# Kernel tuning notes

Measured on AMD Instinct MI355X. Metric: run time of the kernel, lower is better.

The kernel has to match this reference:

```python
import jax, jax.numpy as jnp
import numpy as np

B, M, PAST, FUT, NPRED, D = 512, 32768, 8, 12, 20, 48


def _gru_step(h, x, w_ih, w_hh, b_ih, b_hh):
    # torch GRU cell: gates ordered [r, z, n]
    gi = x @ w_ih.T + b_ih
    gh = h @ w_hh.T + b_hh
    ir, iz, inn = jnp.split(gi, 3, axis=-1)
    hr, hz, hn = jnp.split(gh, 3, axis=-1)
    r = jax.nn.sigmoid(ir + hr)
    z = jax.nn.sigmoid(iz + hz)
    n = jnp.tanh(inn + r * hn)
    return (1.0 - z) * n + z * h


def setup_inputs() -> dict:
    key = jax.random.key(0)
    ks = jax.random.split(key, 16)
    f32 = jnp.float32
    def rn(k, shp, sc):
        return (jax.random.normal(k, shp, dtype=f32) * sc)
    return {
        "past": jax.random.normal(ks[0], (B, PAST, 2), dtype=f32),
        "obs_traj": jax.random.normal(ks[1], (B, PAST, 2), dtype=f32),
        "conv_w": rn(ks[2], (D, 2, 3), 0.3),
        "conv_b": jnp.zeros((D,), f32),
        "enc_w_ih": rn(ks[3], (3 * D, D), 0.1),
        "enc_w_hh": rn(ks[4], (3 * D, D), 0.1),
        "enc_b_ih": jnp.zeros((3 * D,), f32),
        "enc_b_hh": jnp.zeros((3 * D,), f32),
        "memory_past": jax.random.normal(ks[5], (M, D), dtype=f32),
        "memory_fut": jax.random.normal(ks[6], (M, D), dtype=f32),
        "Wq": rn(ks[7], (D, D), 0.1), "bq": jnp.zeros((D,), f32),
        "Wk": rn(ks[8], (D, D), 0.1), "bk": jnp.zeros((D,), f32),
        "Wv": rn(ks[9], (D, D), 0.1), "bv": jnp.zeros((D,), f32),
        "dec_w_ih": rn(ks[10], (6 * D, 2 * D), 0.1),
        "dec_w_hh": rn(ks[11], (6 * D, 2 * D), 0.1),
        "dec_b_ih": jnp.zeros((6 * D,), f32),
        "dec_b_hh": jnp.zeros((6 * D,), f32),
        "fc_w": rn(ks[12], (2, 2 * D), 0.1),
        "fc_b": jnp.zeros((2,), f32),
    }


def reference(past, obs_traj, conv_w, conv_b, enc_w_ih, enc_w_hh, enc_b_ih, enc_b_hh,
              memory_past, memory_fut, Wq, bq, Wk, bk, Wv, bv,
              dec_w_ih, dec_w_hh, dec_b_ih, dec_b_hh, fc_w, fc_b):
    b = past.shape[0]
    # --- past encoder: Conv1d(2,48,3,pad=1) + ReLU, then GRU(48,48) ---
    x = jnp.transpose(past, (0, 2, 1))                     # [B,2,T]
    emb = jax.lax.conv_general_dilated(
        x, conv_w, (1,), [(1, 1)], dimension_numbers=("NCH", "OIH", "NCH"))
    emb = jax.nn.relu(emb + conv_b[None, :, None])         # [B,48,T]
    emb = jnp.transpose(emb, (2, 0, 1))                    # [T,B,48] for scan

    def enc_step(h, x_t):
        return _gru_step(h, x_t, enc_w_ih, enc_w_hh, enc_b_ih, enc_b_hh), None
    state_past, _ = jax.lax.scan(enc_step, jnp.zeros((b, D), past.dtype), emb)  # [B,48]

    # --- iterative refinement: 20 rounds of attention over the full memory ---
    # Lin_K/Lin_V are applied to the same (full) banks every iteration -> hoist.
    K = memory_past @ Wk.T + bk                            # [M,48]
    V = memory_fut @ Wv.T + bv                             # [M,48]

    def irm_step(c, _):
        q = c @ Wq.T + bq                                  # [B,48]
        a = jax.nn.softmax(q @ K.T, axis=-1)               # [B,M], scale=1.0
        att = a @ V                                        # [B,48]
        return q + att, att
    _, atts = jax.lax.scan(irm_step, state_past, None, length=NPRED)  # [20,B,48]
    pred = jnp.transpose(atts, (1, 0, 2)).reshape(-1, D)   # [B*20,48] (b-major)

    # --- GRU(96,96) decoder, future_len steps, input only at t=0 ---
    n = b * NPRED
    present = jnp.repeat(obs_traj[:, -1], NPRED, axis=0)   # [B*20,2]
    sp = jnp.repeat(state_past, NPRED, axis=0)             # [B*20,48]
    info = jnp.concatenate([sp, pred], axis=1)             # [B*20,96]
    xs = jnp.concatenate(
        [info[None], jnp.zeros((FUT - 1, n, 2 * D), info.dtype)], axis=0)

    def dec_step(carry, x_t):
        h, pres = carry
        h = _gru_step(h, x_t, dec_w_ih, dec_w_hh, dec_b_ih, dec_b_hh)
        pres = pres + (h @ fc_w.T + fc_b)
        return (h, pres), pres
    _, coords = jax.lax.scan(
        dec_step, (jnp.zeros((n, 2 * D), info.dtype), present), xs)  # [FUT,B*20,2]

    prediction = jnp.transpose(coords, (1, 0, 2)).reshape(b, NPRED, FUT, 2)
    return prediction
```

## Files before the change

kernel.cpp:

```cpp
#include <hip/hip_runtime.h>

typedef unsigned short u16;
typedef unsigned int u32;
typedef __attribute__((ext_vector_type(8))) short short8v;
typedef __attribute__((ext_vector_type(4))) float f32x4;

#define GLD_LDS(g, l) __builtin_amdgcn_global_load_lds( \
    (const __attribute__((address_space(1))) void*)(g), \
    (__attribute__((address_space(3))) void*)(l), 16, 0, 0)

#define LOG2E 1.44269504f

__device__ __forceinline__ u16 f2bf(float f){
  union { float f; u32 u; } v; v.f = f;
  u32 r = v.u + 0x7FFFu + ((v.u >> 16) & 1u);
  return (u16)(r >> 16);
}
__device__ __forceinline__ float bf2f(u16 h){
  union { u32 u; float f; } v; v.u = ((u32)h) << 16;
  return v.f;
}
__device__ __forceinline__ u32 pk2(float a, float b){
  union { float f; u32 u; } x, y; x.f = a; y.f = b;
  return __builtin_amdgcn_perm(y.u + 0x8000u, x.u + 0x8000u, 0x07060302u);
}
__device__ __forceinline__ float sigm(float x){ return 1.f/(1.f+__expf(-x)); }
__device__ __forceinline__ float tanh_fast(float x){ return 1.f - 2.f/(1.f+__expf(2.f*x)); }

__global__ void prep_kernel(const float* dih, const float* dhh,
    const float* eih, const float* ehh, const float* wq, const float* wk, const float* wv,
    u16* Dih, u16* Dhh, u16* Eih, u16* Ehh, u16* Qf, u16* Kf, u16* Vf)
{
  int idx = blockIdx.x*256 + threadIdx.x;
// ... 161 lines not shown
      short8v aF1 = *(const short8v*)&smf[ln*72 + 32 + qd*8];
      f32x4 k3[3], v3[3];
      #pragma unroll
      for (int nt = 0; nt < 3; ++nt){ k3[nt] = zf; v3[nt] = zf; }
      #pragma unroll
      for (int nt = 0; nt < 3; ++nt){
        k3[nt] = __builtin_amdgcn_mfma_f32_16x16x32_bf16(aP0, *(const short8v*)&sWkF[((nt*2+0)*4+qd)*128 + ln*8], k3[nt], 0,0,0);
        k3[nt] = __builtin_amdgcn_mfma_f32_16x16x32_bf16(aP1, *(const short8v*)&sWkF[((nt*2+1)*4+qd)*128 + ln*8], k3[nt], 0,0,0);
        v3[nt] = __builtin_amdgcn_mfma_f32_16x16x32_bf16(aF0, *(const short8v*)&sWvF[((nt*2+0)*4+qd)*128 + ln*8], v3[nt], 0,0,0);
        v3[nt] = __builtin_amdgcn_mfma_f32_16x16x32_bf16(aF1, *(const short8v*)&sWvF[((nt*2+1)*4+qd)*128 + ln*8], v3[nt], 0,0,0);
      }
      for (int i = lane; i < 128; i += 64) ((u32*)sKT)[(wid*16 + (i>>3))*32 + 24 + (i&7)] = 0;
      #pragma unroll
      for (int nt = 0; nt < 3; ++nt)
        #pragma unroll
        for (int r = 0; r < 4; ++r){
          int keyl = wid*16 + qd*4 + r, d = nt*16 + ln;
          sKT[keyl*64 + d] = f2bf(k3[nt][r] + bkv[nt]);
          sVT[d*72 + keyl] = f2bf(v3[nt][r] + bvv[nt]);
        }
      __syncthreads();
      for (int i = tid; i < 512; i += 256)
        *(uint4*)((char*)(Kb + (size_t)tile*64*64) + i*16) = *(const uint4*)((char*)sKT + i*16);
      for (int i = tid; i < 384; i += 256){
        int d = i>>3, sub = i&7;
        *(uint4*)((char*)(Vc + ((size_t)((tile*64)>>8)*48 + d)*256 + ((tile*64)&255)) + sub*16)
            = *(const uint4*)((char*)sVT + d*144 + sub*16);
      }
      __syncthreads();
    }
  }
}

__global__ __launch_bounds__(256, 1) void iter_kernel(int mode, int it,
    const u16* qbB, const u16* Kb, const u16* Vc, const u16* WqF, const float* bq,
    const float* qfP, float* qfC, float* pred,
    const float* mP, const float* lP, const float* aP,
    float* mC, float* lC, float* aC)
{
  __shared__ __align__(16) char SMEM[55936];
  u16*   sQ  = (u16*)(SMEM + 45056);
  float* sWc = (float*)(SMEM + 49152);
  float* sLg = (float*)(SMEM + 51200);
  u16*   sCb = (u16*)(SMEM + 51332);
  const int tid = threadIdx.x, bx = blockIdx.x;
  const int wid = tid>>6, lane = tid&63, qd = lane>>4, ln = lane&15;
  const int rg = bx>>4, ch = bx&15;
  const int rowbase = rg*32;
  f32x4 zf = {0.f,0.f,0.f,0.f};

  if (mode == 1){
    float* sRed = (float*)SMEM;
    {
      int row = tid>>3, jj = tid&7, grow = rowbase + row;
      float m0 = mP[grow*16 + jj*2], m1 = mP[grow*16 + jj*2+1];
      float l0 = lP[grow*16 + jj*2], l1 = lP[grow*16 + jj*2+1];
      float mg = fmaxf(m0, m1);
      #pragma unroll
      for (int k = 1; k < 8; k <<= 1) mg = fmaxf(mg, __shfl_xor(mg, k));
      float w0 = exp2f(m0 - mg), w1 = exp2f(m1 - mg);
      float wl = w0*l0 + w1*l1;
      #pragma unroll
      for (int k = 1; k < 8; k <<= 1) wl += __shfl_xor(wl, k);
      sWc[row*16 + jj*2] = w0; sWc[row*16 + jj*2+1] = w1;
      if (jj == 0) sLg[row] = wl;
    }
    __syncthreads();
    {
      f32x4 accv[6];
      #pragma unroll
      for (int i = 0; i < 6; ++i) accv[i] = zf;
      #pragma unroll
      for (int ci = 0; ci < 4; ++ci){
        int c = wid*4 + ci;
        const f32x4* slab = (const f32x4*)(aP + ((size_t)c*512 + rowbase)*48);
        #pragma unroll
        for (int i = 0; i < 6; ++i){
          f32x4 v = slab[i*64 + lane];
          int rr = (i*64 + lane)/12;
          float w = sWc[rr*16 + c];
          accv[i][0] += w*v[0]; accv[i][1] += w*v[1];
          accv[i][2] += w*v[2]; accv[i][3] += w*v[3];
        }
      }
      float* red = sRed + wid*1536;
      #pragma unroll
      for (int i = 0; i < 6; ++i)
        *(f32x4*)&red[(i*64 + lane)*4] = accv[i];
    }
    __syncthreads();
    {
      int row = tid>>3, jj = tid&7, grow = rowbase + row;
      float lg = sLg[row];
      int base = row*48 + jj*6;
      #pragma unroll
      for (int d6 = 0; d6 < 6; ++d6){
        int d = jj*6 + d6;
        float s = sRed[base+d6] + sRed[1536+base+d6] + sRed[3072+base+d6] + sRed[4608+base+d6];
        float a = s / lg;
        if (ch == 0) pred[(size_t)(grow*20 + (it-1))*48 + d] = a;
        sCb[row*72 + d] = f2bf(qfP[grow*48 + d] + a);
      }
      ((u32*)&sCb[row*72 + 48])[jj] = 0;
    }
    __syncthreads();
    if (wid < 2){
      short8v ac0 = *(const short8v*)&sCb[(wid*16+ln)*72 + qd*8];
      short8v ac1 = *(const short8v*)&sCb[(wid*16+ln)*72 + 32 + qd*8];
      f32x4 q3[3];
      #pragma unroll
      for (int nt = 0; nt < 3; ++nt){
        q3[nt] = zf;
        q3[nt] = __builtin_amdgcn_mfma_f32_16x16x32_bf16(ac0, *(const short8v*)&WqF[((nt*2+0)*4+qd)*128 + ln*8], q3[nt], 0,0,0);
        q3[nt] = __builtin_amdgcn_mfma_f32_16x16x32_bf16(ac1, *(const short8v*)&WqF[((nt*2+1)*4+qd)*128 + ln*8], q3[nt], 0,0,0);
      }
      #pragma unroll
      for (int nt = 0; nt < 3; ++nt)
        #pragma unroll
        for (int r = 0; r < 4; ++r){
          int lr = wid*16 + qd*4 + r, d = nt*16 + ln;
          float v = q3[nt][r] + bq[d];
          if (ch == 0) qfC[(rowbase + lr)*48 + d] = v;
          sQ[lr*64 + d] = f2bf(v * LOG2E);
        }
    } else {
      for (int i = tid-128; i < 256; i += 128){
        int r2 = i>>3, p = i&7;
        ((u32*)&sQ[r2*64 + 48])[p] = 0;
      }
    }
    __syncthreads();
  } else {
    const u32* src = (const u32*)(qbB + rowbase*64);
    ((u32*)sQ)[tid]       = src[tid];
    ((u32*)sQ)[256 + tid] = src[256 + tid];
    ((u32*)sQ)[512 + tid] = src[512 + tid];
    ((u32*)sQ)[768 + tid] = src[768 + tid];
    __syncthreads();
  }

  const int wslice = ch*2048 + wid*512;
  u16* sp8 = (u16*)(SMEM + 26624);
  short8v aq[2][2];
  #pragma unroll
  for (int rt = 0; rt < 2; ++rt)
    #pragma unroll
    for (int kc = 0; kc < 2; ++kc)
      aq[rt][kc] = *(const short8v*)&sQ[(rt*16+ln)*64 + kc*32 + qd*8];
  f32x4 acc[2][3];
  #pragma unroll
  for (int rt = 0; rt < 2; ++rt) for (int dt = 0; dt < 3; ++dt) acc[rt][dt] = zf;
  float mrun[2] = {-3.0e38f, -3.0e38f}, lrun[2] = {0.f, 0.f};
  u16* spb[2] = { sp8 + (wid*2+0)*1152, sp8 + (wid*2+1)*1152 };

  #pragma unroll
  for (int kt = 0; kt < 8; ++kt){
    const int tb = wslice + kt*64;
    const u16* kb = Kb + (size_t)tb*64;
    const u16* vb = Vc + (size_t)(tb>>8)*48*256 + (tb & 255);
    short8v kf[4][2], vf[2][3];
    #pragma unroll
    for (int nt = 0; nt < 4; ++nt)
      #pragma unroll
      for (int kc = 0; kc < 2; ++kc)
        kf[nt][kc] = *(const short8v*)&kb[(nt*16+ln)*64 + kc*32 + qd*8];
    #pragma unroll
    for (int kc = 0; kc < 2; ++kc)
      #pragma unroll
      for (int dt = 0; dt < 3; ++dt)
        vf[kc][dt] = *(const short8v*)&vb[(dt*16+ln)*256 + kc*32 + qd*8];
    f32x4 s[2][4];
    #pragma unroll
    for (int rt = 0; rt < 2; ++rt)
      #pragma unroll
      for (int nt = 0; nt < 4; ++nt){
        f32x4 z = zf;
        z = __builtin_amdgcn_mfma_f32_16x16x32_bf16(kf[nt][0], aq[rt][0], z, 0,0,0);
        z = __builtin_amdgcn_mfma_f32_16x16x32_bf16(kf[nt][1], aq[rt][1], z, 0,0,0);
        s[rt][nt] = z;
      }
    #pragma unroll
    for (int rt = 0; rt < 2; ++rt){
      float vmax = fmaxf(fmaxf(fmaxf(s[rt][0][0], s[rt][0][1]), fmaxf(s[rt][0][2], s[rt][0][3])),
                   fmaxf(fmaxf(s[rt][1][0], s[rt][1][1]), fmaxf(s[rt][1][2], s[rt][1][3])));
      vmax = fmaxf(vmax, fmaxf(fmaxf(fmaxf(s[rt][2][0], s[rt][2][1]), fmaxf(s[rt][2][2], s[rt][2][3])),
                   fmaxf(fmaxf(s[rt][3][0], s[rt][3][1]), fmaxf(s[rt][3][2], s[rt][3][3]))));
      vmax = fmaxf(vmax, __shfl_xor(vmax, 16));
      vmax = fmaxf(vmax, __shfl_xor(vmax, 32));
      float mnew = fmaxf(mrun[rt], vmax);
      float alpha = exp2f(mrun[rt] - mnew);
      mrun[rt] = mnew;
      u16* sp = spb[rt];
      float lsum = 0.f;
      #pragma unroll
      for (int nt = 0; nt < 4; ++nt){
        float p0 = exp2f(s[rt][nt][0]-mnew), p1 = exp2f(s[rt][nt][1]-mnew);
        float p2 = exp2f(s[rt][nt][2]-mnew), p3 = exp2f(s[rt][nt][3]-mnew);
        lsum += (p0+p1)+(p2+p3);
        uint2 pk; pk.x = pk2(p0,p1); pk.y = pk2(p2,p3);
        *(uint2*)&sp[ln*72 + nt*16 + qd*4] = pk;
      }
      lsum += __shfl_xor(lsum, 16);
      lsum += __shfl_xor(lsum, 32);
      lrun[rt] = lrun[rt]*alpha + lsum;
      #pragma unroll
      for (int dt = 0; dt < 3; ++dt){
        acc[rt][dt][0] *= alpha; acc[rt][dt][1] *= alpha;
        acc[rt][dt][2] *= alpha; acc[rt][dt][3] *= alpha;
      }
      short8v pb0 = *(const short8v*)&sp[ln*72 + qd*8];
      short8v pb1 = *(const short8v*)&sp[ln*72 + 32 + qd*8];
      #pragma unroll
      for (int dt = 0; dt < 3; ++dt){
        acc[rt][dt] = __builtin_amdgcn_mfma_f32_16x16x32_bf16(vf[0][dt], pb0, acc[rt][dt], 0,0,0);
        acc[rt][dt] = __builtin_amdgcn_mfma_f32_16x16x32_bf16(vf[1][dt], pb1, acc[rt][dt], 0,0,0);
      }
    }
  }
  __syncthreads();
  float* sMg = (float*)SMEM;
  #pragma unroll
  for (int rt = 0; rt < 2; ++rt)
    #pragma unroll
    for (int dt = 0; dt < 3; ++dt)
      #pragma unroll
      for (int r = 0; r < 4; ++r)
        sMg[wid*1600 + (rt*16+ln)*50 + dt*16 + qd*4 + r] = acc[rt][dt][r];
  if (lane < 16){
    sMg[wid*1600 + ln*50 + 48] = mrun[0]; sMg[wid*1600 + ln*50 + 49] = lrun[0];
    sMg[wid*1600 + (16+ln)*50 + 48] = mrun[1]; sMg[wid*1600 + (16+ln)*50 + 49] = lrun[1];
  }
  __syncthreads();
  {
    int row = tid>>3, jj = tid&7, grow = rowbase + row;
    float m0 = sMg[row*50+48], m1 = sMg[1600+row*50+48];
    float m2 = sMg[3200+row*50+48], m3 = sMg[4800+row*50+48];
    float mg = fmaxf(fmaxf(m0,m1), fmaxf(m2,m3));
    float e0 = exp2f(m0-mg), e1 = exp2f(m1-mg), e2 = exp2f(m2-mg), e3 = exp2f(m3-mg);
    float lg = e0*sMg[row*50+49] + e1*sMg[1600+row*50+49]
             + e2*sMg[3200+row*50+49] + e3*sMg[4800+row*50+49];
    if (jj == 0){ mC[grow*16 + ch] = mg; lC[grow*16 + ch] = lg; }
    int d0 = jj*6;
    #pragma unroll
    for (int d6 = 0; d6 < 6; ++d6){
      int d = d0 + d6;
      aC[((size_t)ch*512 + grow)*48 + d] =
          e0*sMg[row*50+d] + e1*sMg[1600+row*50+d]
        + e2*sMg[3200+row*50+d] + e3*sMg[4800+row*50+d];
    }
  }
}

__global__ __launch_bounds__(384, 1) void dec_kernel(
    const u16* Dihf, const u16* Dhhf, const float* b_ih, const float* b_hh,
    const float* stateP, const float* pred, const float* obs,
    const float* mF, const float* lF, const float* aF,
    const float* fc_w, const float* fc_b, float* out)
{
  __shared__ __align__(16) u16 sx[2][16*106];
  __shared__ float sPx[2][6][16], sPy[2][6][16];
  const int tid = threadIdx.x, bx = blockIdx.x;
  const int wid = tid>>6, lane = tid&63, qd = lane>>4, ln = lane&15;
  const int rw = bx*16;
  f32x4 zf = {0.f,0.f,0.f,0.f};

  for (int i = tid; i < 1536; i += 384){
    int r = i/96, k = i - r*96;
    int row = rw + r, b20 = row/20;
    float v = (k < 48) ? stateP[b20*48 + k] : pred[(size_t)row*48 + (k-48)];
    sx[0][r*106 + k] = f2bf(v);
  }
  if (tid < 48){
    int r19 = (19 - (rw % 20)) % 20;
    if (r19 < 16){
      int b = (rw + r19)/20;
      float mg = -3.0e38f, mv[16];
      #pragma unroll
      for (int c = 0; c < 16; ++c){ mv[c] = mF[b*16 + c]; mg = fmaxf(mg, mv[c]); }
      float num = 0.f, den = 0.f;
      #pragma unroll
      for (int c = 0; c < 16; ++c){
        float w = exp2f(mv[c] - mg);
        den += w * lF[b*16 + c];
        num += w * aF[((size_t)c*512 + b)*48 + tid];
      }
      sx[0][r19*106 + 48 + tid] = f2bf(num/den);
    }
  }
  short8v whh[3][3];
  #pragma unroll
  for (int g = 0; g < 3; ++g)
    #pragma unroll
    for (int kc = 0; kc < 3; ++kc)
      whh[g][kc] = *(const short8v*)&Dhhf[(((g*6+wid)*3+kc)*4+qd)*128 + ln*8];
  const int d = wid*16 + ln;
  float biR=b_ih[d], biZ=b_ih[96+d], biN=b_ih[192+d];
  float bhR=b_hh[d], bhZ=b_hh[96+d], bhN=b_hh[192+d];
  float fw0=fc_w[d], fw1=fc_w[96+d];
  float hold[4] = {0.f,0.f,0.f,0.f};
  float fcb0 = fc_b[0], fcb1 = fc_b[1];
  float pres0 = 0.f, pres1 = 0.f;
  if (wid == 0 && lane < 16){
    int b20 = (rw + lane)/20;
    pres0 = obs[b20*16 + 14];
    pres1 = obs[b20*16 + 15];
  }
  __syncthreads();

  #pragma unroll 1
  for (int t = 0; t < 12; ++t){
    const u16* sr = sx[t&1];
    u16* sw = sx[(t+1)&1];
    short8v xa0 = *(const short8v*)&sr[ln*106 + qd*8];
    short8v xa1 = *(const short8v*)&sr[ln*106 + 32 + qd*8];
    short8v xa2 = *(const short8v*)&sr[ln*106 + 64 + qd*8];
    f32x4 acc[3] = {zf, zf, zf};
    if (t == 0){
      #pragma unroll
      for (int g = 0; g < 3; ++g){
        int nt = g*6 + wid;
        acc[g] = __builtin_amdgcn_mfma_f32_16x16x32_bf16(xa0, *(const short8v*)&Dihf[((nt*3+0)*4+qd)*128 + ln*8], acc[g], 0,0,0);
        acc[g] = __builtin_amdgcn_mfma_f32_16x16x32_bf16(xa1, *(const short8v*)&Dihf[((nt*3+1)*4+qd)*128 + ln*8], acc[g], 0,0,0);
        acc[g] = __builtin_amdgcn_mfma_f32_16x16x32_bf16(xa2, *(const short8v*)&Dihf[((nt*3+2)*4+qd)*128 + ln*8], acc[g], 0,0,0);
      }
    } else {
      #pragma unroll
      for (int g = 0; g < 3; ++g){
        acc[g] = __builtin_amdgcn_mfma_f32_16x16x32_bf16(xa0, whh[g][0], acc[g], 0,0,0);
        acc[g] = __builtin_amdgcn_mfma_f32_16x16x32_bf16(xa1, whh[g][1], acc[g], 0,0,0);
        acc[g] = __builtin_amdgcn_mfma_f32_16x16x32_bf16(xa2, whh[g][2], acc[g], 0,0,0);
      }
    }
    float px[4], py[4];
    #pragma unroll
    for (int r = 0; r < 4; ++r){
      float rr = sigm(acc[0][r] + biR + bhR);
      float zz = sigm(acc[1][r] + biZ + bhZ);
      float nn = (t == 0) ? tanh_fast(acc[2][r] + biN + rr*bhN)
                          : tanh_fast(biN + rr*(acc[2][r] + bhN));
      float hv = (1.f-zz)*nn + zz*hold[r];
      hold[r] = hv;
      sw[(qd*4+r)*106 + d] = f2bf(hv);
      px[r] = fw0*hv;
      py[r] = fw1*hv;
    }
    #pragma unroll
    for (int msk = 8; msk >= 1; msk >>= 1)
      #pragma unroll
      for (int r = 0; r < 4; ++r){
        px[r] += __shfl_xor(px[r], msk);
        py[r] += __shfl_xor(py[r], msk);
      }
    if (ln == 0){
      #pragma unroll
      for (int r = 0; r < 4; ++r){
        sPx[t&1][wid][qd*4+r] = px[r];
        sPy[t&1][wid][qd*4+r] = py[r];
      }
    }
    __syncthreads();
    if (wid == 0 && lane < 16){
      float fx = 0.f, fy = 0.f;
      #pragma unroll
      for (int w = 0; w < 6; ++w){ fx += sPx[t&1][w][lane]; fy += sPy[t&1][w][lane]; }
      pres0 += fx + fcb0;
      pres1 += fy + fcb1;
      out[((size_t)(rw + lane)*12 + t)*2 + 0] = pres0;
      out[((size_t)(rw + lane)*12 + t)*2 + 1] = pres1;
    }
  }
}

extern "C" void kernel_launch(void* const* d_in, const int* in_sizes, int n_in,
                              void* d_out, int out_size, void* d_ws, size_t ws_size,
                              hipStream_t stream)
{
  const float* past        = (const float*)d_in[0];
  const float* obs         = (const float*)d_in[1];
  const float* conv_w      = (const float*)d_in[2];
  const float* conv_b      = (const float*)d_in[3];
  const float* enc_w_ih    = (const float*)d_in[4];
  const float* enc_w_hh    = (const float*)d_in[5];
  const float* enc_b_ih    = (const float*)d_in[6];
  const float* enc_b_hh    = (const float*)d_in[7];
  const float* memory_past = (const float*)d_in[8];
  const float* memory_fut  = (const float*)d_in[9];
  const float* Wq = (const float*)d_in[10];
  const float* bq = (const float*)d_in[11];
  const float* Wk = (const float*)d_in[12];
  const float* bk = (const float*)d_in[13];
  const float* Wv = (const float*)d_in[14];
  const float* bv = (const float*)d_in[15];
  const float* dec_w_ih = (const float*)d_in[16];
  const float* dec_w_hh = (const float*)d_in[17];
  const float* dec_b_ih = (const float*)d_in[18];
  const float* dec_b_hh = (const float*)d_in[19];
  const float* fc_w = (const float*)d_in[20];
  const float* fc_b = (const float*)d_in[21];
  float* out = (float*)d_out;

  char* ws = (char*)d_ws;
  size_t off = 0;
  auto alloc = [&](size_t bytes){ void* p = ws + off; off += (bytes + 255) & ~(size_t)255; return p; };
  float* stateP = (float*)alloc(512*48*4);
  float* qfA    = (float*)alloc(512*48*4);
  float* qfB    = (float*)alloc(512*48*4);
  u16*   qbB    = (u16*)alloc(512*64*2);
  float* mB[2], *lB[2], *aB[2];
  for (int i = 0; i < 2; ++i){
    mB[i] = (float*)alloc(512*16*4);
    lB[i] = (float*)alloc(512*16*4);
    aB[i] = (float*)alloc((size_t)512*16*48*4);
  }
  float* pred = (float*)alloc((size_t)10240*48*4);
  u16*   Kb   = (u16*)alloc((size_t)32768*64*2);
  u16*   Vc   = (u16*)alloc((size_t)32768*48*2);
  u16*   Dihf = (u16*)alloc(27648*2);
  u16*   Dhhf = (u16*)alloc(27648*2);
  u16*   EihF = (u16*)alloc(9216*2);
  u16*   EhhF = (u16*)alloc(9216*2);
  u16*   WqF  = (u16*)alloc(3072*2);
  u16*   WkF  = (u16*)alloc(3072*2);
  u16*   WvF  = (u16*)alloc(3072*2);
  float* qbuf[2] = { qfA, qfB };

  prep_kernel<<<324, 256, 0, stream>>>(dec_w_ih, dec_w_hh, enc_w_ih, enc_w_hh,
                                       Wq, Wk, Wv, Dihf, Dhhf, EihF, EhhF, WqF, WkF, WvF);

  setup_kernel<<<512, 256, 0, stream>>>(
      past, conv_w, conv_b, enc_b_ih, enc_b_hh, memory_past, memory_fut,
      bq, bk, bv, EihF, EhhF, WqF, WkF, WvF,
      stateP, qfA, qbB, Kb, Vc);

  iter_kernel<<<256, 256, 0, stream>>>(0, 0, qbB, Kb, Vc, WqF, bq,
      qfA, qfA, pred, mB[1], lB[1], aB[1], mB[0], lB[0], aB[0]);
  for (int it = 1; it < 20; ++it){
    int pv = (it-1)&1, cu = it&1;
    iter_kernel<<<256, 256, 0, stream>>>(1, it, qbB, Kb, Vc, WqF, bq,
        qbuf[pv], qbuf[cu], pred, mB[pv], lB[pv], aB[pv], mB[cu], lB[cu], aB[cu]);
  }

  dec_kernel<<<640, 384, 0, stream>>>(Dihf, Dhhf, dec_b_ih, dec_b_hh,
      stateP, pred, obs, mB[1], lB[1], aB[1], fc_w, fc_b, out);
}
```

Before: 628.7 us.

## Run decoder GRU with one wavefront per block and remap attention chunk order

The decoder kernel moves from six wavefronts per 16-row block, which needed shared-memory reduction of the fc projection and a second sync, to a single wavefront that computes all 18 gate tiles itself. The fc reduction and trajectory accumulation now stay in registers. Weights are read from global memory every step instead of being cached in registers, and each block does six times the serial MFMA work with fewer waves for latency hiding. Separately, the iteration kernel's chunk index is permuted across block IDs, likely to change how blocks are spread over XCDs or caches.

```diff
diff --git a/kernel.cpp b/kernel.cpp
--- a/kernel.cpp
+++ b/kernel.cpp
@@ -239,7 +239,8 @@
   u16*   sCb = (u16*)(SMEM + 51332);
   const int tid = threadIdx.x, bx = blockIdx.x;
   const int wid = tid>>6, lane = tid&63, qd = lane>>4, ln = lane&15;
-  const int rg = bx>>4, ch = bx&15;
+  const int ch = (bx&7)*2 + ((bx>>3)&1);
+  const int rg = bx>>4;
   const int rowbase = rg*32;
   f32x4 zf = {0.f,0.f,0.f,0.f};
 
@@ -445,26 +446,25 @@
   }
 }
 
-__global__ __launch_bounds__(384, 1) void dec_kernel(
+__global__ __launch_bounds__(64) void dec_kernel(
     const u16* Dihf, const u16* Dhhf, const float* b_ih, const float* b_hh,
     const float* stateP, const float* pred, const float* obs,
     const float* mF, const float* lF, const float* aF,
     const float* fc_w, const float* fc_b, float* out)
 {
   __shared__ __align__(16) u16 sx[2][16*106];
-  __shared__ float sPx[2][6][16], sPy[2][6][16];
-  const int tid = threadIdx.x, bx = blockIdx.x;
-  const int wid = tid>>6, lane = tid&63, qd = lane>>4, ln = lane&15;
+  const int lane = threadIdx.x, bx = blockIdx.x;
+  const int qd = lane>>4, ln = lane&15;
   const int rw = bx*16;
   f32x4 zf = {0.f,0.f,0.f,0.f};
 
-  for (int i = tid; i < 1536; i += 384){
+  for (int i = lane; i < 1536; i += 64){
     int r = i/96, k = i - r*96;
     int row = rw + r, b20 = row/20;
     float v = (k < 48) ? stateP[b20*48 + k] : pred[(size_t)row*48 + (k-48)];
     sx[0][r*106 + k] = f2bf(v);
   }
-  if (tid < 48){
+  if (lane < 48){
     int r19 = (19 - (rw % 20)) % 20;
     if (r19 < 16){
       int b = (rw + r19)/20;
@@ -476,28 +476,29 @@
       for (int c = 0; c < 16; ++c){
         float w = exp2f(mv[c] - mg);
         den += w * lF[b*16 + c];
-        num += w * aF[((size_t)c*512 + b)*48 + tid];
-      }
-      sx[0][r19*106 + 48 + tid] = f2bf(num/den);
-    }
-  }
-  short8v whh[3][3];
+        num += w * aF[((size_t)c*512 + b)*48 + lane];
+      }
+      sx[0][r19*106 + 48 + lane] = f2bf(num/den);
+    }
+  }
+  float biR[6],biZ[6],biN[6],bhR[6],bhZ[6],bhN[6],fw0[6],fw1[6];
   #pragma unroll
-  for (int g = 0; g < 3; ++g)
-    #pragma unroll
-    for (int kc = 0; kc < 3; ++kc)
-      whh[g][kc] = *(const short8v*)&Dhhf[(((g*6+wid)*3+kc)*4+qd)*128 + ln*8];
-  const int d = wid*16 + ln;
-  float biR=b_ih[d], biZ=b_ih[96+d], biN=b_ih[192+d];
-  float bhR=b_hh[d], bhZ=b_hh[96+d], bhN=b_hh[192+d];
-  float fw0=fc_w[d], fw1=fc_w[96+d];
-  float hold[4] = {0.f,0.f,0.f,0.f};
+  for (int i = 0; i < 6; ++i){
+    int d = i*16 + ln;
+    biR[i]=b_ih[d]; biZ[i]=b_ih[96+d]; biN[i]=b_ih[192+d];
+    bhR[i]=b_hh[d]; bhZ[i]=b_hh[96+d]; bhN[i]=b_hh[192+d];
+    fw0[i]=fc_w[d]; fw1[i]=fc_w[96+d];
+  }
+  float hold[6][4];
+  #pragma unroll
+  for (int i = 0; i < 6; ++i) for (int r = 0; r < 4; ++r) hold[i][r] = 0.f;
   float fcb0 = fc_b[0], fcb1 = fc_b[1];
-  float pres0 = 0.f, pres1 = 0.f;
-  if (wid == 0 && lane < 16){
-    int b20 = (rw + lane)/20;
-    pres0 = obs[b20*16 + 14];
-    pres1 = obs[b20*16 + 15];
+  float pres0[4], pres1[4];
+  #pragma unroll
+  for (int r = 0; r < 4; ++r){
+    int b20 = (rw + qd*4 + r)/20;
+    pres0[r] = obs[b20*16 + 14];
+    pres1[r] = obs[b20*16 + 15];
   }
   __syncthreads();
 
@@ -508,36 +509,32 @@
     short8v xa0 = *(const short8v*)&sr[ln*106 + qd*8];
     short8v xa1 = *(const short8v*)&sr[ln*106 + 32 + qd*8];
     short8v xa2 = *(const short8v*)&sr[ln*106 + 64 + qd*8];
-    f32x4 acc[3] = {zf, zf, zf};
-    if (t == 0){
-      #pragma unroll
-      for (int g = 0; g < 3; ++g){
-        int nt = g*6 + wid;
-        acc[g] = __builtin_amdgcn_mfma_f32_16x16x32_bf16(xa0, *(const short8v*)&Dihf[((nt*3+0)*4+qd)*128 + ln*8], acc[g], 0,0,0);
-        acc[g] = __builtin_amdgcn_mfma_f32_16x16x32_bf16(xa1, *(const short8v*)&Dihf[((nt*3+1)*4+qd)*128 + ln*8], acc[g], 0,0,0);
-        acc[g] = __builtin_amdgcn_mfma_f32_16x16x32_bf16(xa2, *(const short8v*)&Dihf[((nt*3+2)*4+qd)*128 + ln*8], acc[g], 0,0,0);
-      }
-    } else {
-      #pragma unroll
-      for (int g = 0; g < 3; ++g){
-        acc[g] = __builtin_amdgcn_mfma_f32_16x16x32_bf16(xa0, whh[g][0], acc[g], 0,0,0);
-        acc[g] = __builtin_amdgcn_mfma_f32_16x16x32_bf16(xa1, whh[g][1], acc[g], 0,0,0);
-        acc[g] = __builtin_amdgcn_mfma_f32_16x16x32_bf16(xa2, whh[g][2], acc[g], 0,0,0);
-      }
-    }
-    float px[4], py[4];
-    #pragma unroll
-    for (int r = 0; r < 4; ++r){
-      float rr = sigm(acc[0][r] + biR + bhR);
-      float zz = sigm(acc[1][r] + biZ + bhZ);
-      float nn = (t == 0) ? tanh_fast(acc[2][r] + biN + rr*bhN)
-                          : tanh_fast(biN + rr*(acc[2][r] + bhN));
-      float hv = (1.f-zz)*nn + zz*hold[r];
-      hold[r] = hv;
-      sw[(qd*4+r)*106 + d] = f2bf(hv);
-      px[r] = fw0*hv;
-      py[r] = fw1*hv;
-    }
+    const u16* W = (t == 0) ? Dihf : Dhhf;
+    f32x4 acc[18];
+    #pragma unroll
+    for (int i = 0; i < 18; ++i) acc[i] = zf;
+    #pragma unroll
+    for (int nt = 0; nt < 18; ++nt){
+      acc[nt] = __builtin_amdgcn_mfma_f32_16x16x32_bf16(xa0, *(const short8v*)&W[((nt*3+0)*4+qd)*128 + ln*8], acc[nt], 0,0,0);
+      acc[nt] = __builtin_amdgcn_mfma_f32_16x16x32_bf16(xa1, *(const short8v*)&W[((nt*3+1)*4+qd)*128 + ln*8], acc[nt], 0,0,0);
+      acc[nt] = __builtin_amdgcn_mfma_f32_16x16x32_bf16(xa2, *(const short8v*)&W[((nt*3+2)*4+qd)*128 + ln*8], acc[nt], 0,0,0);
+    }
+    float px[4] = {0,0,0,0}, py[4] = {0,0,0,0};
+    #pragma unroll
+    for (int r = 0; r < 4; ++r)
+      #pragma unroll
+      for (int i = 0; i < 6; ++i){
+        int d = i*16 + ln;
+        float rr = sigm(acc[i][r]   + biR[i] + bhR[i]);
+        float zz = sigm(acc[i+6][r] + biZ[i] + bhZ[i]);
+        float nn = (t == 0) ? tanh_fast(acc[i+12][r] + biN[i] + rr*bhN[i])
+                            : tanh_fast(biN[i] + rr*(acc[i+12][r] + bhN[i]));
+        float hv = (1.f-zz)*nn + zz*hold[i][r];
+        hold[i][r] = hv;
+        sw[(qd*4+r)*106 + d] = f2bf(hv);
+        px[r] += fw0[i]*hv;
+        py[r] += fw1[i]*hv;
+      }
     #pragma unroll
     for (int msk = 8; msk >= 1; msk >>= 1)
       #pragma unroll
@@ -545,23 +542,20 @@
         px[r] += __shfl_xor(px[r], msk);
         py[r] += __shfl_xor(py[r], msk);
       }
+    #pragma unroll
+    for (int r = 0; r < 4; ++r){
+      pres0[r] += px[r] + fcb0;
+      pres1[r] += py[r] + fcb1;
+    }
     if (ln == 0){
       #pragma unroll
       for (int r = 0; r < 4; ++r){
-        sPx[t&1][wid][qd*4+r] = px[r];
-        sPy[t&1][wid][qd*4+r] = py[r];
+        int row = rw + qd*4 + r;
+        out[((size_t)row*12 + t)*2 + 0] = pres0[r];
+        out[((size_t)row*12 + t)*2 + 1] = pres1[r];
       }
     }
     __syncthreads();
-    if (wid == 0 && lane < 16){
-      float fx = 0.f, fy = 0.f;
-      #pragma unroll
-      for (int w = 0; w < 6; ++w){ fx += sPx[t&1][w][lane]; fy += sPy[t&1][w][lane]; }
-      pres0 += fx + fcb0;
-      pres1 += fy + fcb1;
-      out[((size_t)(rw + lane)*12 + t)*2 + 0] = pres0;
-      out[((size_t)(rw + lane)*12 + t)*2 + 1] = pres1;
-    }
   }
 }
 
@@ -634,6 +628,6 @@
         qbuf[pv], qbuf[cu], pred, mB[pv], lB[pv], aB[pv], mB[cu], lB[cu], aB[cu]);
   }
 
-  dec_kernel<<<640, 384, 0, stream>>>(Dihf, Dhhf, dec_b_ih, dec_b_hh,
+  dec_kernel<<<640, 64, 0, stream>>>(Dihf, Dhhf, dec_b_ih, dec_b_hh,
       stateP, pred, obs, mB[1], lB[1], aB[1], fc_w, fc_b, out);
 }
```

New measurement: 639.0 us. No clear change (+1.6%).

## Fuse 20 attention iteration launches into one cooperative kernel with grid sync

Applied to the files above, without the earlier changes.

Replaces the 20 back-to-back iter_kernel launches with a single cooperative launch that loops over iterations and uses grid-wide sync between them. The query state now stays in shared memory across iterations. The goal is to remove per-launch overhead and launch gaps. A fallback path runs the per-iteration launches if the cooperative launch fails. It also changes the dec_kernel LDS row stride from 106 to 104 and drops its min-blocks launch bound, which may affect bank conflicts and occupancy.

```diff
diff --git a/kernel.cpp b/kernel.cpp
--- a/kernel.cpp
+++ b/kernel.cpp
@@ -1,4 +1,7 @@
 #include <hip/hip_runtime.h>
+#include <hip/hip_cooperative_groups.h>
+
+namespace cg = cooperative_groups;
 
 typedef unsigned short u16;
 typedef unsigned int u32;
@@ -226,232 +229,251 @@
   }
 }
 
-__global__ __launch_bounds__(256, 1) void iter_kernel(int mode, int it,
-    const u16* qbB, const u16* Kb, const u16* Vc, const u16* WqF, const float* bq,
-    const float* qfP, float* qfC, float* pred,
-    const float* mP, const float* lP, const float* aP,
-    float* mC, float* lC, float* aC)
+__global__ __launch_bounds__(256, 1) void iter_kernel(int it0, int it1,
+    const u16* Kb, const u16* Vc, const u16* WqF, const float* bq,
+    const float* qfIn, float* qfA, float* qfB, float* pred,
+    float* m0b, float* l0b, float* a0b, float* m1b, float* l1b, float* a1b)
 {
-  __shared__ __align__(16) char SMEM[55936];
+  __shared__ __align__(16) char SMEM[62080];
   u16*   sQ  = (u16*)(SMEM + 45056);
   float* sWc = (float*)(SMEM + 49152);
   float* sLg = (float*)(SMEM + 51200);
   u16*   sCb = (u16*)(SMEM + 51332);
+  float* sQf = (float*)(SMEM + 55936);
   const int tid = threadIdx.x, bx = blockIdx.x;
   const int wid = tid>>6, lane = tid&63, qd = lane>>4, ln = lane&15;
   const int rg = bx>>4, ch = bx&15;
   const int rowbase = rg*32;
   f32x4 zf = {0.f,0.f,0.f,0.f};
 
-  if (mode == 1){
-    float* sRed = (float*)SMEM;
-    {
-      int row = tid>>3, jj = tid&7, grow = rowbase + row;
-      float m0 = mP[grow*16 + jj*2], m1 = mP[grow*16 + jj*2+1];
-      float l0 = lP[grow*16 + jj*2], l1 = lP[grow*16 + jj*2+1];
-      float mg = fmaxf(m0, m1);
-      #pragma unroll
-      for (int k = 1; k < 8; k <<= 1) mg = fmaxf(mg, __shfl_xor(mg, k));
-      float w0 = exp2f(m0 - mg), w1 = exp2f(m1 - mg);
-      float wl = w0*l0 + w1*l1;
-      #pragma unroll
-      for (int k = 1; k < 8; k <<= 1) wl += __shfl_xor(wl, k);
-      sWc[row*16 + jj*2] = w0; sWc[row*16 + jj*2+1] = w1;
-      if (jj == 0) sLg[row] = wl;
+  for (int i = tid; i < 1536; i += 256){
+    float v = qfIn[rowbase*48 + i];
+    sQf[i] = v;
+    int row = i/48, d = i - row*48;
+    sQ[row*64 + d] = f2bf(v * LOG2E);
+  }
+  { int r2 = tid>>3, p = tid&7; ((u32*)sQ)[r2*32 + 24 + p] = 0; }
+  __syncthreads();
+
+  #pragma unroll 1
+  for (int it = it0; it < it1; ++it){
+    const float* mP = (it&1) ? m0b : m1b;
+    const float* lP = (it&1) ? l0b : l1b;
+    const float* aP = (it&1) ? a0b : a1b;
+    float* mC = (it&1) ? m1b : m0b;
+    float* lC = (it&1) ? l1b : l0b;
+    float* aC = (it&1) ? a1b : a0b;
+    float* qOut = (it&1) ? qfB : qfA;
+
+    if (it > 0){
+      float* sRed = (float*)SMEM;
+      {
+        int row = tid>>3, jj = tid&7, grow = rowbase + row;
+        float m0 = mP[grow*16 + jj*2], m1 = mP[grow*16 + jj*2+1];
+        float l0 = lP[grow*16 + jj*2], l1 = lP[grow*16 + jj*2+1];
+        float mg = fmaxf(m0, m1);
+        #pragma unroll
+        for (int k = 1; k < 8; k <<= 1) mg = fmaxf(mg, __shfl_xor(mg, k));
+        float w0 = exp2f(m0 - mg), w1 = exp2f(m1 - mg);
+        float wl = w0*l0 + w1*l1;
+        #pragma unroll
+        for (int k = 1; k < 8; k <<= 1) wl += __shfl_xor(wl, k);
+        sWc[row*16 + jj*2] = w0; sWc[row*16 + jj*2+1] = w1;
+        if (jj == 0) sLg[row] = wl;
+      }
+      __syncthreads();
+      {
+        f32x4 accv[6];
+        #pragma unroll
+        for (int i = 0; i < 6; ++i) accv[i] = zf;
+        #pragma unroll
+        for (int ci = 0; ci < 4; ++ci){
+          int c = wid*4 + ci;
+          const f32x4* slab = (const f32x4*)(aP + ((size_t)c*512 + rowbase)*48);
+          #pragma unroll
+          for (int i = 0; i < 6; ++i){
+            f32x4 v = slab[i*64 + lane];
+            int rr = (i*64 + lane)/12;
+            float w = sWc[rr*16 + c];
+            accv[i][0] += w*v[0]; accv[i][1] += w*v[1];
+            accv[i][2] += w*v[2]; accv[i][3] += w*v[3];
+          }
+        }
+        float* red = sRed + wid*1536;
+        #pragma unroll
+        for (int i = 0; i < 6; ++i)
+          *(f32x4*)&red[(i*64 + lane)*4] = accv[i];
+      }
+      __syncthreads();
+      {
+        int row = tid>>3, jj = tid&7, grow = rowbase + row;
+        float lg = sLg[row];
+        int base = row*48 + jj*6;
+        #pragma unroll
+        for (int d6 = 0; d6 < 6; ++d6){
+          int d = jj*6 + d6;
+          float s = sRed[base+d6] + sRed[1536+base+d6] + sRed[3072+base+d6] + sRed[4608+base+d6];
+          float a = s / lg;
+          if (ch == 0) pred[(size_t)(grow*20 + (it-1))*48 + d] = a;
+          sCb[row*72 + d] = f2bf(sQf[row*48 + d] + a);
+        }
+        ((u32*)&sCb[row*72 + 48])[jj] = 0;
+      }
+      __syncthreads();
+      if (wid < 2){
+        short8v ac0 = *(const short8v*)&sCb[(wid*16+ln)*72 + qd*8];
+        short8v ac1 = *(const short8v*)&sCb[(wid*16+ln)*72 + 32 + qd*8];
+        f32x4 q3[3];
+        #pragma unroll
+        for (int nt = 0; nt < 3; ++nt){
+          q3[nt] = zf;
+          q3[nt] = __builtin_amdgcn_mfma_f32_16x16x32_bf16(ac0, *(const short8v*)&WqF[((nt*2+0)*4+qd)*128 + ln*8], q3[nt], 0,0,0);
+          q3[nt] = __builtin_amdgcn_mfma_f32_16x16x32_bf16(ac1, *(const short8v*)&WqF[((nt*2+1)*4+qd)*128 + ln*8], q3[nt], 0,0,0);
+        }
+        #pragma unroll
+        for (int nt = 0; nt < 3; ++nt)
+          #pragma unroll
+          for (int r = 0; r < 4; ++r){
+            int lr = wid*16 + qd*4 + r, d = nt*16 + ln;
+            float v = q3[nt][r] + bq[d];
+            sQf[lr*48 + d] = v;
+            if (ch == 0) qOut[(rowbase + lr)*48 + d] = v;
+            sQ[lr*64 + d] = f2bf(v * LOG2E);
+          }
+      } else {
+        for (int i = tid-128; i < 256; i += 128){
+          int r2 = i>>3, p = i&7;
+          ((u32*)&sQ[r2*64 + 48])[p] = 0;
+        }
+      }
+      __syncthreads();
+    }
+
+    const int wslice = ch*2048 + wid*512;
+    u16* sp8 = (u16*)(SMEM + 26624);
+    short8v aq[2][2];
+    #pragma unroll
+    for (int rt = 0; rt < 2; ++rt)
+      #pragma unroll
+      for (int kc = 0; kc < 2; ++kc)
+        aq[rt][kc] = *(const short8v*)&sQ[(rt*16+ln)*64 + kc*32 + qd*8];
+    f32x4 acc[2][3];
+    #pragma unroll
+    for (int rt = 0; rt < 2; ++rt) for (int dt = 0; dt < 3; ++dt) acc[rt][dt] = zf;
+    float mrun[2] = {-3.0e38f, -3.0e38f}, lrun[2] = {0.f, 0.f};
+    u16* spb[2] = { sp8 + (wid*2+0)*1152, sp8 + (wid*2+1)*1152 };
+
+    #pragma unroll
+    for (int kt = 0; kt < 8; ++kt){
+      const int tb = wslice + kt*64;
+      const u16* kb = Kb + (size_t)tb*64;
+      const u16* vb = Vc + (size_t)(tb>>8)*48*256 + (tb & 255);
+      short8v kf[4][2], vf[2][3];
+      #pragma unroll
+      for (int nt = 0; nt < 4; ++nt)
+        #pragma unroll
+        for (int kc = 0; kc < 2; ++kc)
+          kf[nt][kc] = *(const short8v*)&kb[(nt*16+ln)*64 + kc*32 + qd*8];
+      #pragma unroll
+      for (int kc = 0; kc < 2; ++kc)
+        #pragma unroll
+        for (int dt = 0; dt < 3; ++dt)
+          vf[kc][dt] = *(const short8v*)&vb[(dt*16+ln)*256 + kc*32 + qd*8];
+      f32x4 s[2][4];
+      #pragma unroll
+      for (int rt = 0; rt < 2; ++rt)
+        #pragma unroll
+        for (int nt = 0; nt < 4; ++nt){
+          f32x4 z = zf;
+          z = __builtin_amdgcn_mfma_f32_16x16x32_bf16(kf[nt][0], aq[rt][0], z, 0,0,0);
+          z = __builtin_amdgcn_mfma_f32_16x16x32_bf16(kf[nt][1], aq[rt][1], z, 0,0,0);
+          s[rt][nt] = z;
+        }
+      #pragma unroll
+      for (int rt = 0; rt < 2; ++rt){
+        float vmax = fmaxf(fmaxf(fmaxf(s[rt][0][0], s[rt][0][1]), fmaxf(s[rt][0][2], s[rt][0][3])),
+                     fmaxf(fmaxf(s[rt][1][0], s[rt][1][1]), fmaxf(s[rt][1][2], s[rt][1][3])));
+        vmax = fmaxf(vmax, fmaxf(fmaxf(fmaxf(s[rt][2][0], s[rt][2][1]), fmaxf(s[rt][2][2], s[rt][2][3])),
+                     fmaxf(fmaxf(s[rt][3][0], s[rt][3][1]), fmaxf(s[rt][3][2], s[rt][3][3]))));
+        vmax = fmaxf(vmax, __shfl_xor(vmax, 16));
+        vmax = fmaxf(vmax, __shfl_xor(vmax, 32));
+        float mnew = fmaxf(mrun[rt], vmax);
+        float alpha = exp2f(mrun[rt] - mnew);
+        mrun[rt] = mnew;
+        u16* sp = spb[rt];
+        float lsum = 0.f;
+        #pragma unroll
+        for (int nt = 0; nt < 4; ++nt){
+          float p0 = exp2f(s[rt][nt][0]-mnew), p1 = exp2f(s[rt][nt][1]-mnew);
+          float p2 = exp2f(s[rt][nt][2]-mnew), p3 = exp2f(s[rt][nt][3]-mnew);
+          lsum += (p0+p1)+(p2+p3);
+          uint2 pk; pk.x = pk2(p0,p1); pk.y = pk2(p2,p3);
+          *(uint2*)&sp[ln*72 + nt*16 + qd*4] = pk;
+        }
+        lsum += __shfl_xor(lsum, 16);
+        lsum += __shfl_xor(lsum, 32);
+        lrun[rt] = lrun[rt]*alpha + lsum;
+        #pragma unroll
+        for (int dt = 0; dt < 3; ++dt){
+          acc[rt][dt][0] *= alpha; acc[rt][dt][1] *= alpha;
+          acc[rt][dt][2] *= alpha; acc[rt][dt][3] *= alpha;
+        }
+        short8v pb0 = *(const short8v*)&sp[ln*72 + qd*8];
+        short8v pb1 = *(const short8v*)&sp[ln*72 + 32 + qd*8];
+        #pragma unroll
+        for (int dt = 0; dt < 3; ++dt){
+          acc[rt][dt] = __builtin_amdgcn_mfma_f32_16x16x32_bf16(vf[0][dt], pb0, acc[rt][dt], 0,0,0);
+          acc[rt][dt] = __builtin_amdgcn_mfma_f32_16x16x32_bf16(vf[1][dt], pb1, acc[rt][dt], 0,0,0);
+        }
+      }
     }
     __syncthreads();
-    {
-      f32x4 accv[6];
-      #pragma unroll
-      for (int i = 0; i < 6; ++i) accv[i] = zf;
-      #pragma unroll
-      for (int ci = 0; ci < 4; ++ci){
-        int c = wid*4 + ci;
-        const f32x4* slab = (const f32x4*)(aP + ((size_t)c*512 + rowbase)*48);
-        #pragma unroll
-        for (int i = 0; i < 6; ++i){
-          f32x4 v = slab[i*64 + lane];
-          int rr = (i*64 + lane)/12;
-          float w = sWc[rr*16 + c];
-          accv[i][0] += w*v[0]; accv[i][1] += w*v[1];
-          accv[i][2] += w*v[2]; accv[i][3] += w*v[3];
-        }
-      }
-      float* red = sRed + wid*1536;
-      #pragma unroll
-      for (int i = 0; i < 6; ++i)
-        *(f32x4*)&red[(i*64 + lane)*4] = accv[i];
+    float* sMg = (float*)SMEM;
+    #pragma unroll
+    for (int rt = 0; rt < 2; ++rt)
+      #pragma unroll
+      for (int dt = 0; dt < 3; ++dt)
+        #pragma unroll
+        for (int r = 0; r < 4; ++r)
+          sMg[wid*1600 + (rt*16+ln)*50 + dt*16 + qd*4 + r] = acc[rt][dt][r];
+    if (lane < 16){
+      sMg[wid*1600 + ln*50 + 48] = mrun[0]; sMg[wid*1600 + ln*50 + 49] = lrun[0];
+      sMg[wid*1600 + (16+ln)*50 + 48] = mrun[1]; sMg[wid*1600 + (16+ln)*50 + 49] = lrun[1];
     }
     __syncthreads();
     {
       int row = tid>>3, jj = tid&7, grow = rowbase + row;
-      float lg = sLg[row];
-      int base = row*48 + jj*6;
+      float m0 = sMg[row*50+48], m1 = sMg[1600+row*50+48];
+      float m2 = sMg[3200+row*50+48], m3 = sMg[4800+row*50+48];
+      float mg = fmaxf(fmaxf(m0,m1), fmaxf(m2,m3));
+      float e0 = exp2f(m0-mg), e1 = exp2f(m1-mg), e2 = exp2f(m2-mg), e3 = exp2f(m3-mg);
+      float lg = e0*sMg[row*50+49] + e1*sMg[1600+row*50+49]
+               + e2*sMg[3200+row*50+49] + e3*sMg[4800+row*50+49];
+      if (jj == 0){ mC[grow*16 + ch] = mg; lC[grow*16 + ch] = lg; }
+      int d0 = jj*6;
       #pragma unroll
       for (int d6 = 0; d6 < 6; ++d6){
-        int d = jj*6 + d6;
-        float s = sRed[base+d6] + sRed[1536+base+d6] + sRed[3072+base+d6] + sRed[4608+base+d6];
-        float a = s / lg;
-        if (ch == 0) pred[(size_t)(grow*20 + (it-1))*48 + d] = a;
-        sCb[row*72 + d] = f2bf(qfP[grow*48 + d] + a);
-      }
-      ((u32*)&sCb[row*72 + 48])[jj] = 0;
+        int d = d0 + d6;
+        aC[((size_t)ch*512 + grow)*48 + d] =
+            e0*sMg[row*50+d] + e1*sMg[1600+row*50+d]
+          + e2*sMg[3200+row*50+d] + e3*sMg[4800+row*50+d];
+      }
     }
     __syncthreads();
-    if (wid < 2){
-      short8v ac0 = *(const short8v*)&sCb[(wid*16+ln)*72 + qd*8];
-      short8v ac1 = *(const short8v*)&sCb[(wid*16+ln)*72 + 32 + qd*8];
-      f32x4 q3[3];
-      #pragma unroll
-      for (int nt = 0; nt < 3; ++nt){
-        q3[nt] = zf;
-        q3[nt] = __builtin_amdgcn_mfma_f32_16x16x32_bf16(ac0, *(const short8v*)&WqF[((nt*2+0)*4+qd)*128 + ln*8], q3[nt], 0,0,0);
-        q3[nt] = __builtin_amdgcn_mfma_f32_16x16x32_bf16(ac1, *(const short8v*)&WqF[((nt*2+1)*4+qd)*128 + ln*8], q3[nt], 0,0,0);
-      }
-      #pragma unroll
-      for (int nt = 0; nt < 3; ++nt)
-        #pragma unroll
-        for (int r = 0; r < 4; ++r){
-          int lr = wid*16 + qd*4 + r, d = nt*16 + ln;
-          float v = q3[nt][r] + bq[d];
-          if (ch == 0) qfC[(rowbase + lr)*48 + d] = v;
-          sQ[lr*64 + d] = f2bf(v * LOG2E);
-        }
-    } else {
-      for (int i = tid-128; i < 256; i += 128){
-        int r2 = i>>3, p = i&7;
-        ((u32*)&sQ[r2*64 + 48])[p] = 0;
-      }
-    }
-    __syncthreads();
-  } else {
-    const u32* src = (const u32*)(qbB + rowbase*64);
-    ((u32*)sQ)[tid]       = src[tid];
-    ((u32*)sQ)[256 + tid] = src[256 + tid];
-    ((u32*)sQ)[512 + tid] = src[512 + tid];
-    ((u32*)sQ)[768 + tid] = src[768 + tid];
-    __syncthreads();
-  }
-
-  const int wslice = ch*2048 + wid*512;
-  u16* sp8 = (u16*)(SMEM + 26624);
-  short8v aq[2][2];
-  #pragma unroll
-  for (int rt = 0; rt < 2; ++rt)
-    #pragma unroll
-    for (int kc = 0; kc < 2; ++kc)
-      aq[rt][kc] = *(const short8v*)&sQ[(rt*16+ln)*64 + kc*32 + qd*8];
-  f32x4 acc[2][3];
-  #pragma unroll
-  for (int rt = 0; rt < 2; ++rt) for (int dt = 0; dt < 3; ++dt) acc[rt][dt] = zf;
-  float mrun[2] = {-3.0e38f, -3.0e38f}, lrun[2] = {0.f, 0.f};
-  u16* spb[2] = { sp8 + (wid*2+0)*1152, sp8 + (wid*2+1)*1152 };
-
-  #pragma unroll
-  for (int kt = 0; kt < 8; ++kt){
-    const int tb = wslice + kt*64;
-    const u16* kb = Kb + (size_t)tb*64;
-    const u16* vb = Vc + (size_t)(tb>>8)*48*256 + (tb & 255);
-    short8v kf[4][2], vf[2][3];
-    #pragma unroll
-    for (int nt = 0; nt < 4; ++nt)
-      #pragma unroll
-      for (int kc = 0; kc < 2; ++kc)
-        kf[nt][kc] = *(const short8v*)&kb[(nt*16+ln)*64 + kc*32 + qd*8];
-    #pragma unroll
-    for (int kc = 0; kc < 2; ++kc)
-      #pragma unroll
-      for (int dt = 0; dt < 3; ++dt)
-        vf[kc][dt] = *(const short8v*)&vb[(dt*16+ln)*256 + kc*32 + qd*8];
-    f32x4 s[2][4];
-    #pragma unroll
-    for (int rt = 0; rt < 2; ++rt)
-      #pragma unroll
-      for (int nt = 0; nt < 4; ++nt){
-        f32x4 z = zf;
-        z = __builtin_amdgcn_mfma_f32_16x16x32_bf16(kf[nt][0], aq[rt][0], z, 0,0,0);
-        z = __builtin_amdgcn_mfma_f32_16x16x32_bf16(kf[nt][1], aq[rt][1], z, 0,0,0);
-        s[rt][nt] = z;
-      }
-    #pragma unroll
-    for (int rt = 0; rt < 2; ++rt){
-      float vmax = fmaxf(fmaxf(fmaxf(s[rt][0][0], s[rt][0][1]), fmaxf(s[rt][0][2], s[rt][0][3])),
-                   fmaxf(fmaxf(s[rt][1][0], s[rt][1][1]), fmaxf(s[rt][1][2], s[rt][1][3])));
-      vmax = fmaxf(vmax, fmaxf(fmaxf(fmaxf(s[rt][2][0], s[rt][2][1]), fmaxf(s[rt][2][2], s[rt][2][3])),
-                   fmaxf(fmaxf(s[rt][3][0], s[rt][3][1]), fmaxf(s[rt][3][2], s[rt][3][3]))));
-      vmax = fmaxf(vmax, __shfl_xor(vmax, 16));
-      vmax = fmaxf(vmax, __shfl_xor(vmax, 32));
-      float mnew = fmaxf(mrun[rt], vmax);
-      float alpha = exp2f(mrun[rt] - mnew);
-      mrun[rt] = mnew;
-      u16* sp = spb[rt];
-      float lsum = 0.f;
-      #pragma unroll
-      for (int nt = 0; nt < 4; ++nt){
-        float p0 = exp2f(s[rt][nt][0]-mnew), p1 = exp2f(s[rt][nt][1]-mnew);
-        float p2 = exp2f(s[rt][nt][2]-mnew), p3 = exp2f(s[rt][nt][3]-mnew);
-        lsum += (p0+p1)+(p2+p3);
-        uint2 pk; pk.x = pk2(p0,p1); pk.y = pk2(p2,p3);
-        *(uint2*)&sp[ln*72 + nt*16 + qd*4] = pk;
-      }
-      lsum += __shfl_xor(lsum, 16);
-      lsum += __shfl_xor(lsum, 32);
-      lrun[rt] = lrun[rt]*alpha + lsum;
-      #pragma unroll
-      for (int dt = 0; dt < 3; ++dt){
-        acc[rt][dt][0] *= alpha; acc[rt][dt][1] *= alpha;
-        acc[rt][dt][2] *= alpha; acc[rt][dt][3] *= alpha;
-      }
-      short8v pb0 = *(const short8v*)&sp[ln*72 + qd*8];
-      short8v pb1 = *(const short8v*)&sp[ln*72 + 32 + qd*8];
-      #pragma unroll
-      for (int dt = 0; dt < 3; ++dt){
-        acc[rt][dt] = __builtin_amdgcn_mfma_f32_16x16x32_bf16(vf[0][dt], pb0, acc[rt][dt], 0,0,0);
-        acc[rt][dt] = __builtin_amdgcn_mfma_f32_16x16x32_bf16(vf[1][dt], pb1, acc[rt][dt], 0,0,0);
-      }
-    }
-  }
-  __syncthreads();
-  float* sMg = (float*)SMEM;
-  #pragma unroll
-  for (int rt = 0; rt < 2; ++rt)
-    #pragma unroll
-    for (int dt = 0; dt < 3; ++dt)
-      #pragma unroll
-      for (int r = 0; r < 4; ++r)
-        sMg[wid*1600 + (rt*16+ln)*50 + dt*16 + qd*4 + r] = acc[rt][dt][r];
-  if (lane < 16){
-    sMg[wid*1600 + ln*50 + 48] = mrun[0]; sMg[wid*1600 + ln*50 + 49] = lrun[0];
-    sMg[wid*1600 + (16+ln)*50 + 48] = mrun[1]; sMg[wid*1600 + (16+ln)*50 + 49] = lrun[1];
-  }
-  __syncthreads();
-  {
-    int row = tid>>3, jj = tid&7, grow = rowbase + row;
-    float m0 = sMg[row*50+48], m1 = sMg[1600+row*50+48];
-    float m2 = sMg[3200+row*50+48], m3 = sMg[4800+row*50+48];
-    float mg = fmaxf(fmaxf(m0,m1), fmaxf(m2,m3));
-    float e0 = exp2f(m0-mg), e1 = exp2f(m1-mg), e2 = exp2f(m2-mg), e3 = exp2f(m3-mg);
-    float lg = e0*sMg[row*50+49] + e1*sMg[1600+row*50+49]
-             + e2*sMg[3200+row*50+49] + e3*sMg[4800+row*50+49];
-    if (jj == 0){ mC[grow*16 + ch] = mg; lC[grow*16 + ch] = lg; }
-    int d0 = jj*6;
-    #pragma unroll
-    for (int d6 = 0; d6 < 6; ++d6){
-      int d = d0 + d6;
-      aC[((size_t)ch*512 + grow)*48 + d] =
-          e0*sMg[row*50+d] + e1*sMg[1600+row*50+d]
-        + e2*sMg[3200+row*50+d] + e3*sMg[4800+row*50+d];
-    }
-  }
-}
-
-__global__ __launch_bounds__(384, 1) void dec_kernel(
+    if (it + 1 < it1){
+      __threadfence();
+      cg::this_grid().sync();
+    }
+  }
+}
+
+__global__ __launch_bounds__(384) void dec_kernel(
     const u16* Dihf, const u16* Dhhf, const float* b_ih, const float* b_hh,
     const float* stateP, const float* pred, const float* obs,
     const float* mF, const float* lF, const float* aF,
     const float* fc_w, const float* fc_b, float* out)
 {
-  __shared__ __align__(16) u16 sx[2][16*106];
+  __shared__ __align__(16) u16 sx[2][16*104];
   __shared__ float sPx[2][6][16], sPy[2][6][16];
   const int tid = threadIdx.x, bx = blockIdx.x;
   const int wid = tid>>6, lane = tid&63, qd = lane>>4, ln = lane&15;
@@ -462,7 +484,7 @@
     int r = i/96, k = i - r*96;
     int row = rw + r, b20 = row/20;
     float v = (k < 48) ? stateP[b20*48 + k] : pred[(size_t)row*48 + (k-48)];
-    sx[0][r*106 + k] = f2bf(v);
+    sx[0][r*104 + k] = f2bf(v);
   }
   if (tid < 48){
     int r19 = (19 - (rw % 20)) % 20;
@@ -478,7 +500,7 @@
         den += w * lF[b*16 + c];
         num += w * aF[((size_t)c*512 + b)*48 + tid];
       }
-      sx[0][r19*106 + 48 + tid] = f2bf(num/den);
+      sx[0][r19*104 + 48 + tid] = f2bf(num/den);
     }
   }
   short8v whh[3][3];
@@ -505,9 +527,9 @@
   for (int t = 0; t < 12; ++t){
     const u16* sr = sx[t&1];
     u16* sw = sx[(t+1)&1];
-    short8v xa0 = *(const short8v*)&sr[ln*106 + qd*8];
-    short8v xa1 = *(const short8v*)&sr[ln*106 + 32 + qd*8];
-    short8v xa2 = *(const short8v*)&sr[ln*106 + 64 + qd*8];
+    short8v xa0 = *(const short8v*)&sr[ln*104 + qd*8];
+    short8v xa1 = *(const short8v*)&sr[ln*104 + 32 + qd*8];
+    short8v xa2 = *(const short8v*)&sr[ln*104 + 64 + qd*8];
     f32x4 acc[3] = {zf, zf, zf};
     if (t == 0){
       #pragma unroll
@@ -534,7 +556,7 @@
                           : tanh_fast(biN + rr*(acc[2][r] + bhN));
       float hv = (1.f-zz)*nn + zz*hold[r];
       hold[r] = hv;
-      sw[(qd*4+r)*106 + d] = f2bf(hv);
+      sw[(qd*4+r)*104 + d] = f2bf(hv);
       px[r] = fw0*hv;
       py[r] = fw1*hv;
     }
@@ -600,12 +622,12 @@
   float* qfA    = (float*)alloc(512*48*4);
   float* qfB    = (float*)alloc(512*48*4);
   u16*   qbB    = (u16*)alloc(512*64*2);
-  float* mB[2], *lB[2], *aB[2];
-  for (int i = 0; i < 2; ++i){
-    mB[i] = (float*)alloc(512*16*4);
-    lB[i] = (float*)alloc(512*16*4);
-    aB[i] = (float*)alloc((size_t)512*16*48*4);
-  }
+  float* m0b = (float*)alloc(512*16*4);
+  float* l0b = (float*)alloc(512*16*4);
+  float* a0b = (float*)alloc((size_t)512*16*48*4);
+  float* m1b = (float*)alloc(512*16*4);
+  float* l1b = (float*)alloc(512*16*4);
+  float* a1b = (float*)alloc((size_t)512*16*48*4);
   float* pred = (float*)alloc((size_t)10240*48*4);
   u16*   Kb   = (u16*)alloc((size_t)32768*64*2);
   u16*   Vc   = (u16*)alloc((size_t)32768*48*2);
@@ -616,7 +638,6 @@
   u16*   WqF  = (u16*)alloc(3072*2);
   u16*   WkF  = (u16*)alloc(3072*2);
   u16*   WvF  = (u16*)alloc(3072*2);
-  float* qbuf[2] = { qfA, qfB };
 
   prep_kernel<<<324, 256, 0, stream>>>(dec_w_ih, dec_w_hh, enc_w_ih, enc_w_hh,
                                        Wq, Wk, Wv, Dihf, Dhhf, EihF, EhhF, WqF, WkF, WvF);
@@ -626,14 +647,26 @@
       bq, bk, bv, EihF, EhhF, WqF, WkF, WvF,
       stateP, qfA, qbB, Kb, Vc);
 
-  iter_kernel<<<256, 256, 0, stream>>>(0, 0, qbB, Kb, Vc, WqF, bq,
-      qfA, qfA, pred, mB[1], lB[1], aB[1], mB[0], lB[0], aB[0]);
-  for (int it = 1; it < 20; ++it){
-    int pv = (it-1)&1, cu = it&1;
-    iter_kernel<<<256, 256, 0, stream>>>(1, it, qbB, Kb, Vc, WqF, bq,
-        qbuf[pv], qbuf[cu], pred, mB[pv], lB[pv], aB[pv], mB[cu], lB[cu], aB[cu]);
+  {
+    int it0 = 0, it1 = 20;
+    const u16* Kb_ = Kb; const u16* Vc_ = Vc; const u16* WqF_ = WqF;
+    const float* bq_ = bq; const float* qin = qfA;
+    float* qfA_ = qfA; float* qfB_ = qfB; float* pred_ = pred;
+    float* m0_ = m0b; float* l0_ = l0b; float* a0_ = a0b;
+    float* m1_ = m1b; float* l1_ = l1b; float* a1_ = a1b;
+    void* args[] = { &it0, &it1, &Kb_, &Vc_, &WqF_, &bq_, &qin,
+                     &qfA_, &qfB_, &pred_, &m0_, &l0_, &a0_, &m1_, &l1_, &a1_ };
+    hipError_t e = hipLaunchCooperativeKernel((const void*)iter_kernel,
+                                              dim3(256), dim3(256), args, 0, stream);
+    if (e != hipSuccess){
+      for (int it = 0; it < 20; ++it){
+        const float* q_in = (it == 0) ? qfA : (((it-1)&1) ? qfB : qfA);
+        iter_kernel<<<256, 256, 0, stream>>>(it, it+1, Kb, Vc, WqF, bq,
+            q_in, qfA, qfB, pred, m0b, l0b, a0b, m1b, l1b, a1b);
+      }
+    }
   }
 
   dec_kernel<<<640, 384, 0, stream>>>(Dihf, Dhhf, dec_b_ih, dec_b_hh,
-      stateP, pred, obs, mB[1], lB[1], aB[1], fc_w, fc_b, out);
-}
+      stateP, pred, obs, m1b, l1b, a1b, fc_w, fc_b, out);
+}
```

Result: slower. 1.756 ms (+179.3%).
